# Kernel tuning notes

Hardware: AMD Instinct MI355X
Metric: run time of the kernel (lower is better)

The kernel has to match this reference:

```python
import jax, jax.numpy as jnp
import numpy as np

CORR = 5          # corr_size (patch_size)
UP = 2            # upsample_param
CH = [512, 1024, 512, 256, 256, 256]
SZ = [64, 32, 16, 8, 4, 2]   # pyramid spatial sizes; UP*2**i upsamples all to 128
B = 2
P = CORR * CORR

def upsample_nearest(x, f):
    # nn.Upsample(scale_factor=f, mode='nearest') for integer f
    return jnp.repeat(jnp.repeat(x, f, axis=2), f, axis=3)

def correlate(f1, f2):
    # spatial_correlation_sample: kernel=1, patch=CORR, stride=1, padding=0, dilation_patch=1
    # out[b, pi*CORR+pj, y, x] = sum_c f1[b,c,y,x] * f2[b,c,y+pi-r,x+pj-r] (zeros out of range)
    r = CORR // 2
    b, c, h, w = f1.shape
    f2p = jnp.pad(f2, ((0, 0), (0, 0), (r, r), (r, r)))
    outs = []
    for pi in range(CORR):
        for pj in range(CORR):
            sh = jax.lax.dynamic_slice(f2p, (0, 0, pi, pj), (b, c, h, w))
            outs.append(jnp.sum(f1 * sh, axis=1))
    return jnp.stack(outs, axis=1)  # [B, P, h, w]

def avgpool(x):
    # AvgPool2d(kernel_size=3, stride=2, padding=1), count_include_pad=True (torch default)
    s = jax.lax.reduce_window(x, 0.0, jax.lax.add, (1, 1, 3, 3), (1, 1, 2, 2), ((0, 0), (0, 0), (1, 1), (1, 1)))
    return s / 9.0

def conv3x3(x, w, b):
    y = jax.lax.conv_general_dilated(x, w, (1, 1), ((1, 1), (1, 1)), dimension_numbers=("NCHW", "OIHW", "NCHW"))
    return y + b[None, :, None, None]

def level_step(feat1, feat2, h_pre, c_pre, w, b, lvl):
    f = UP * (2 ** lvl)
    u1 = upsample_nearest(feat1, f)
    u2 = upsample_nearest(feat2, f)
    corr = jax.nn.leaky_relu(correlate(u1, u2), 0.01)
    # int(log2(up_W / feat_W)) pools; this is <= 6 so only avg_pooling1 is ever used
    for _ in range(int(np.log2(u1.shape[3] // feat1.shape[3]))):
        corr = avgpool(corr)
    gates = conv3x3(jnp.concatenate([corr, h_pre], axis=1), w, b)
    i = jax.nn.sigmoid(gates[:, :P])
    fg = jax.nn.sigmoid(gates[:, P:2 * P])
    o = jax.nn.sigmoid(gates[:, 2 * P:3 * P])
    g = jnp.tanh(gates[:, 3 * P:])
    c_next = fg * c_pre + i * g
    h_next = o * jnp.tanh(c_next)
    return h_next, c_next

def setup_inputs():
    keys = jax.random.split(jax.random.key(0), 40)
    d = {}
    k = 0
    for i in range(6):
        d[f"x{i}"] = jax.random.normal(keys[k], (B, CH[i], SZ[i], SZ[i]), jnp.float32); k += 1
        d[f"xp{i}"] = jax.random.normal(keys[k], (B, CH[i], SZ[i], SZ[i]), jnp.float32); k += 1
        d[f"h{i}"] = jax.random.normal(keys[k], (B, P, SZ[i], SZ[i]), jnp.float32); k += 1
        d[f"c{i}"] = jax.random.normal(keys[k], (B, P, SZ[i], SZ[i]), jnp.float32); k += 1
    for i in range(6):
        d[f"W{i}"] = jax.random.normal(keys[k], (4 * P, 2 * P, 3, 3), jnp.float32) * 0.05; k += 1
        d[f"b{i}"] = jnp.zeros((4 * P,), jnp.float32)
    return d

def reference(x0, x1, x2, x3, x4, x5, xp0, xp1, xp2, xp3, xp4, xp5,
              h0, h1, h2, h3, h4, h5, c0, c1, c2, c3, c4, c5,
              W0, W1, W2, W3, W4, W5, b0, b1, b2, b3, b4, b5):
    xs = [x0, x1, x2, x3, x4, x5]
    xps = [xp0, xp1, xp2, xp3, xp4, xp5]
    hs = [h0, h1, h2, h3, h4, h5]
    cs = [c0, c1, c2, c3, c4, c5]
    Ws = [W0, W1, W2, W3, W4, W5]
    bs = [b0, b1, b2, b3, b4, b5]
    outs = []
    for lvl in range(6):
        h_next, c_next = level_step(xs[lvl], xps[lvl], hs[lvl], cs[lvl], Ws[lvl], bs[lvl], lvl)
        outs.extend([h_next, c_next])
    return tuple(outs)
```

## Files before the change

### kernel.cpp

```cpp
#include <hip/hip_runtime.h>

#define NB 2
#define PP 25
#define NLVL 6

struct Params {
  const float* x1[NLVL];
  const float* x2[NLVL];
  const float* h[NLVL];
  const float* c[NLVL];
  const float* W[NLVL];
  const float* bias[NLVL];
  float* Dpart[NLVL];
  float* D[NLVL];
  float* pooled[NLVL];
  float* WT[NLVL];
  float* hout[NLVL];
  float* cout[NLVL];
};

__device__ __forceinline__ float lrelu(float v) { return v > 0.f ? v : 0.01f * v; }

__global__ __launch_bounds__(256) void repack_kernel(Params pr) {
  const int lvl = blockIdx.y;
  const float* W = pr.W[lvl];
  float* WT = pr.WT[lvl];
  for (int i = blockIdx.x * 256 + threadIdx.x; i < 100 * 450; i += gridDim.x * 256) {
    const int oc = i / 450;
    const int r = i - oc * 450;
    WT[r * 100 + oc] = W[i];
  }
}

__global__ __launch_bounds__(256) void dcorr_kernel(Params pr) {
  static const int SZt[6] = {64, 32, 16, 8, 4, 2};
  static const int CHt[6] = {512, 1024, 512, 256, 256, 256};
  static const int NCH[6] = {16, 16, 4, 1, 1, 1};
  static const int LGQ[6] = {4, 3, 2, 0, 0, 0};
  const int lvl = blockIdx.y;
  const int S = SZt[lvl], C = CHt[lvl], nch = NCH[lvl];
  const int rows = NB * S;
  const int bid = blockIdx.x;
  if (bid >= rows * nch) return;
  const int row = bid / nch;
  const int chunk = bid - row * nch;
  const int b = row / S, yb = row - b * S;
  const int tid = threadIdx.x;
  const size_t nlev = (size_t)NB * S * S * 9;
  float* part = pr.Dpart[lvl] + (size_t)chunk * nlev;

  __shared__ float red[9216];

  if (S >= 16) {
    const int lgq = LGQ[lvl];
    const int xqn = S >> 2;
    const int cgn = 256 >> lgq;
    const int xq = tid & (xqn - 1);
    const int cg = tid >> lgq;
    const int chpc = C / nch;
    const int cpt = chpc / cgn;
    const int xb0 = xq << 2;

    const float* f1b = pr.x1[lvl] + (size_t)b * C * S * S + (size_t)yb * S + xb0;
    const float* f2b = pr.x2[lvl] + (size_t)b * C * S * S;

    float acc[9][4];
#pragma unroll
    for (int jj = 0; jj < 9; ++jj)
#pragma unroll
      for (int j = 0; j < 4; ++j) acc[jj][j] = 0.f;

    const int c0 = chunk * chpc + cg;
    for (int t = 0; t < cpt; ++t) {
      const int cc = c0 + t * cgn;
      const float4 f1 = *(const float4*)(f1b + (size_t)cc * S * S);
      const float f1a[4] = {f1.x, f1.y, f1.z, f1.w};
      const float* p2 = f2b + (size_t)cc * S * S;
#pragma unroll
      for (int dy = 0; dy < 3; ++dy) {
        const int yy = yb + dy - 1;
        if (yy < 0 || yy >= S) continue;
        const float* prow = p2 + (size_t)yy * S;
        const float4 m = *(const float4*)(prow + xb0);
        const float lm = (xb0 > 0) ? prow[xb0 - 1] : 0.f;
        const float rm = (xb0 + 4 < S) ? prow[xb0 + 4] : 0.f;
        const float wl[4] = {lm, m.x, m.y, m.z};
        const float wc[4] = {m.x, m.y, m.z, m.w};
        const float wr[4] = {m.y, m.z, m.w, rm};
#pragma unroll
        for (int j = 0; j < 4; ++j) {
          acc[dy * 3 + 0][j] = fmaf(f1a[j], wl[j], acc[dy * 3 + 0][j]);
          acc[dy * 3 + 1][j] = fmaf(f1a[j], wc[j], acc[dy * 3 + 1][j]);
          acc[dy * 3 + 2][j] = fmaf(f1a[j], wr[j], acc[dy * 3 + 2][j]);
        }
      }
    }

    const int n = S * 9;
#pragma unroll
    for (int jj = 0; jj < 9; ++jj)
#pragma unroll
      for (int j = 0; j < 4; ++j)
        red[cg * n + (xb0 + j) * 9 + jj] = acc[jj][j];
    __syncthreads();
    for (int g = cgn >> 1; g >= 1; g >>= 1) {
      for (int i = tid; i < g * n; i += 256) {
        const int c = i / n, e = i - c * n;
        red[c * n + e] += red[(c + g) * n + e];
      }
      __syncthreads();
    }
    float* out = part + (size_t)(b * S + yb) * S * 9;
    for (int i = tid; i < n; i += 256) out[i] = red[i];
  } else {
    const int lg = (S == 8) ? 3 : ((S == 4) ? 2 : 1);
    const int xb = tid & (S - 1), cg = tid >> lg;
    const int NG = 256 >> lg;
    const int cpt = C / NG;

    const float* f1base = pr.x1[lvl] + (size_t)b * C * S * S + (size_t)yb * S + xb;
    const float* f2base = pr.x2[lvl] + (size_t)b * C * S * S;

    float acc[9];
#pragma unroll
    for (int j = 0; j < 9; ++j) acc[j] = 0.f;

    for (int t = 0; t < cpt; ++t) {
      const int cc = cg + t * NG;
      const float f1 = f1base[(size_t)cc * S * S];
      const float* p2 = f2base + (size_t)cc * S * S;
#pragma unroll
      for (int dy = 0; dy < 3; ++dy) {
        const int yy = yb + dy - 1;
        if (yy < 0 || yy >= S) continue;
        const float* prow = p2 + yy * S;
#pragma unroll
        for (int dx = 0; dx < 3; ++dx) {
          const int xx = xb + dx - 1;
          const float v = (xx >= 0 && xx < S) ? prow[xx] : 0.f;
          acc[dy * 3 + dx] += f1 * v;
        }
      }
    }

#pragma unroll
    for (int j = 0; j < 9; ++j) red[tid * 9 + j] = acc[j];
    __syncthreads();
    for (int g = NG >> 1; g >= 1; g >>= 1) {
      if (cg < g) {
#pragma unroll
        for (int j = 0; j < 9; ++j) red[tid * 9 + j] += red[(tid + g * S) * 9 + j];
      }
      __syncthreads();
    }
    if (cg == 0) {
      float* Dp = part + ((size_t)(b * S + yb) * S + xb) * 9;
#pragma unroll
      for (int j = 0; j < 9; ++j) Dp[j] = red[tid * 9 + j];
    }
  }
}

__global__ __launch_bounds__(256) void dreduce_kernel(Params pr) {
  static const int SZt[6] = {64, 32, 16, 8, 4, 2};
  static const int NCH[6] = {16, 16, 4, 1, 1, 1};
  const int lvl = blockIdx.y;
  const int S = SZt[lvl], nch = NCH[lvl];
  const int n = NB * S * S * 9;
  const int i = blockIdx.x * 256 + threadIdx.x;
  if (i >= n) return;
  const float* part = pr.Dpart[lvl];
  float s = 0.f;
  for (int c = 0; c < nch; ++c) s += part[(size_t)c * n + i];
  pr.D[lvl][i] = lrelu(s);
}

__global__ __launch_bounds__(256) void pool_kernel(Params pr) {
  static const int SZt[6] = {64, 32, 16, 8, 4, 2};
  static const int NYC[6] = {8, 4, 2, 1, 1, 1};
  static const int LGS[6] = {6, 5, 4, 3, 2, 1};
  const int lvl = blockIdx.y;
  const int S = SZt[lvl], k = lvl + 1, f = 1 << k, nyc = NYC[lvl], lgS = LGS[lvl];
  const int nyo = S / nyc;
  const int bid = blockIdx.x;
  if (bid >= 50 * nyc) return;
  const int yc = bid / 50;
  const int bp = bid - yc * 50;
  const int b = bp / 25, p = bp - (bp / 25) * 25;
  const int dpy = p / 5 - 2, dpx = p - (p / 5) * 5 - 2;
  const int tid = threadIdx.x;
  const int yo0 = yc * nyo;

  __shared__ float ckb[2][130], clb[2][66];
  __shared__ float Dl[5184];
  __shared__ float tmp[1024];

  if (tid == 0) { ckb[0][0] = 1.f; clb[0][0] = 1.f; }
  __syncthreads();
  int rj = 0, cur = 0;
  for (int j = 0; j < k; ++j) {
    const int half = 1 << j, rn = 2 * half - 1;
    float cknew = 0.f, clnew = 0.f;
    if (tid <= 2 * rn) {
      const int t = tid - rn;
#pragma unroll
      for (int e = -1; e <= 1; ++e) {
        const int u = t + e * half;
        if (u >= -rj && u <= rj) cknew += ckb[cur][u + rj];
      }
      cknew *= (1.f / 3.f);
    }
    if (tid < 2 * half) {
      const int y = tid;
      float s = (y < half) ? clb[cur][y] : 0.f;
      const int u = y - half;
      if (u >= -rj && u <= rj) s += ckb[cur][u + rj];
      clnew = s * (1.f / 3.f);
    }
    __syncthreads();
    if (tid <= 2 * rn) ckb[cur ^ 1][tid] = cknew;
    if (tid < 2 * half) clb[cur ^ 1][tid] = clnew;
    __syncthreads();
    cur ^= 1;
    rj = rn;
  }
  const float* ck = ckb[cur];
  const float* cl = clb[cur];

  const int yb0 = (yo0 > 0) ? yo0 - 1 : 0;
  const int nyb = (yo0 + nyo - 1) - yb0 + 1;
  const float* Dg = pr.D[lvl] + (size_t)b * S * S * 9 + (size_t)yb0 * S * 9;
  const int nload = nyb * S * 9;
  for (int i = tid; i < nload; i += 256) Dl[i] = Dg[i];
  __syncthreads();

  for (int item = tid; item < nyo * 128; item += 256) {
    const int yol = item >> 7, x = item & 127;
    const int yo = yo0 + yol;
    const int xb = x >> k, tx = x & (f - 1);
    const int txp = tx + dpx;
    const int dxi = (txp < 0) ? 0 : ((txp >= f) ? 2 : 1);
    float sum = 0.f;
    if (yo == 0) {
      for (int y = 0; y < f; ++y) {
        const int typ = y + dpy;
        const int dyi = (typ < 0) ? 0 : ((typ >= f) ? 2 : 1);
        sum += cl[y] * Dl[((0 - yb0) * S + xb) * 9 + dyi * 3 + dxi];
      }
    } else {
      const int ylo = yo * f - (f - 1);
      for (int t = 0; t < 2 * f - 1; ++t) {
        const int y = ylo + t;
        const int yb = y >> k, ty = y & (f - 1);
        const int typ = ty + dpy;
        const int dyi = (typ < 0) ? 0 : ((typ >= f) ? 2 : 1);
        sum += ck[t] * Dl[((yb - yb0) * S + xb) * 9 + dyi * 3 + dxi];
      }
    }
    tmp[yol * 128 + x] = sum;
  }
  __syncthreads();

  float* out = pr.pooled[lvl] + (size_t)(b * PP + p) * S * S;
  for (int item = tid; item < nyo * S; item += 256) {
    const int yol = item >> lgS, xo = item & (S - 1);
    float sum = 0.f;
    if (xo == 0) {
      for (int x = 0; x < f; ++x) sum += cl[x] * tmp[yol * 128 + x];
    } else {
      const int xlo = xo * f - (f - 1);
      for (int t = 0; t < 2 * f - 1; ++t) sum += ck[t] * tmp[yol * 128 + xlo + t];
    }
    out[(size_t)(yo0 + yol) * S + xo] = sum;
  }
}

__global__ __launch_bounds__(256) void conv_kernel(Params pr) {
  static const int SZt[6] = {64, 32, 16, 8, 4, 2};
  static const int XTt[6] = {16, 16, 16, 8, 4, 2};
  static const int NXGt[6] = {2, 2, 2, 1, 1, 1};
  const int lvl = blockIdx.y;
  const int S = SZt[lvl], xtile = XTt[lvl], nxg = NXGt[lvl];
  const int nxt = S / xtile;
  const int nblk = NB * S * nxt;
  const int bid = blockIdx.x;
  if (bid >= nblk) return;
  const int b = bid / (S * nxt);
  const int rem = bid - b * (S * nxt);
  const int y = rem / nxt;
  const int xt = rem - y * nxt;
  const int xb0 = xt * xtile;
  const int tid = threadIdx.x;
  const int icc = tid >> 6;
  const int sub = tid & 63;
  const int nact = 25 * nxg;

  __shared__ float lds[7232];

  {
    const float* pooled = pr.pooled[lvl] + (size_t)b * PP * S * S;
    const float* hin = pr.h[lvl] + (size_t)b * PP * S * S;
    for (int i = tid; i < 150 * 20; i += 256) {
      const int r = i / 20, j = i - r * 20;
      const int ky = r / 50, ic = r - ky * 50;
      const int yy = y + ky - 1;
      const int x = xb0 + j - 1;
      float v = 0.f;
      if (yy >= 0 && yy < S && x >= 0 && x < S && j < xtile + 2)
        v = (ic < PP) ? pooled[((size_t)ic * S + yy) * S + x]
                      : hin[((size_t)(ic - PP) * S + yy) * S + x];
      lds[r * 20 + j] = v;
    }
  }
  __syncthreads();

  float acc[4][8];
#pragma unroll
  for (int q = 0; q < 4; ++q)
#pragma unroll
    for (int xx = 0; xx < 8; ++xx) acc[q][xx] = 0.f;

  if (sub < nact) {
    const int xg = sub / 25;
    const int p = sub - xg * 25;
    const int xoff = xg * 8;
    const int ic0 = (icc * 50) >> 2;
    const int ic1 = ((icc + 1) * 50) >> 2;
    const float* wbase = pr.WT[lvl] + p;

    float w[4][9], wn[4][9];
#pragma unroll
    for (int q = 0; q < 4; ++q)
#pragma unroll
      for (int t = 0; t < 9; ++t) w[q][t] = wbase[((size_t)ic0 * 9 + t) * 100 + q * 25];

    for (int ic = ic0; ic < ic1; ++ic) {
      const bool pre = (ic + 1 < ic1);
      if (pre) {
        const float* wq = wbase + (size_t)(ic + 1) * 900;
#pragma unroll
        for (int q = 0; q < 4; ++q)
#pragma unroll
          for (int t = 0; t < 9; ++t) wn[q][t] = wq[t * 100 + q * 25];
      }
#pragma unroll
      for (int ky = 0; ky < 3; ++ky) {
        const float4* rp = (const float4*)(lds + (ky * 50 + ic) * 20 + xoff);
        const float4 A = rp[0], Bv = rp[1], Cv = rp[2];
        const float sg[12] = {A.x, A.y, A.z, A.w, Bv.x, Bv.y, Bv.z, Bv.w,
                              Cv.x, Cv.y, Cv.z, Cv.w};
#pragma unroll
        for (int q = 0; q < 4; ++q) {
          const float w0 = w[q][ky * 3], w1 = w[q][ky * 3 + 1], w2 = w[q][ky * 3 + 2];
#pragma unroll
          for (int xx = 0; xx < 8; ++xx)
            acc[q][xx] = fmaf(w0, sg[xx], fmaf(w1, sg[xx + 1], fmaf(w2, sg[xx + 2], acc[q][xx])));
        }
      }
      if (pre) {
#pragma unroll
        for (int q = 0; q < 4; ++q)
#pragma unroll
          for (int t = 0; t < 9; ++t) w[q][t] = wn[q][t];
      }
    }
  }
  __syncthreads();

  if (sub < nact) {
    float* slot = lds + (icc * 50 + sub) * 36;
#pragma unroll
    for (int q = 0; q < 4; ++q) {
      ((float4*)slot)[q * 2] = make_float4(acc[q][0], acc[q][1], acc[q][2], acc[q][3]);
      ((float4*)slot)[q * 2 + 1] = make_float4(acc[q][4], acc[q][5], acc[q][6], acc[q][7]);
    }
  }
  __syncthreads();

  if (tid < nact) {
    const int xg2 = tid / 25;
    const int p2 = tid - xg2 * 25;
    const int xoff2 = xg2 * 8;

    float g4[4][8];
#pragma unroll
    for (int q = 0; q < 4; ++q)
#pragma unroll
      for (int xx = 0; xx < 8; ++xx) {
        float s = 0.f;
#pragma unroll
        for (int k2 = 0; k2 < 4; ++k2) s += lds[(k2 * 50 + tid) * 36 + q * 8 + xx];
        g4[q][xx] = s;
      }

    const float bi = pr.bias[lvl][p2];
    const float bf = pr.bias[lvl][p2 + 25];
    const float bo = pr.bias[lvl][p2 + 50];
    const float bg = pr.bias[lvl][p2 + 75];
    const size_t base = ((size_t)(b * PP + p2) * S + y) * S + xb0 + xoff2;
    const float* cin = pr.c[lvl] + base;
    float* ho = pr.hout[lvl] + base;
    float* co = pr.cout[lvl] + base;

    float cp[8], hn[8], cn[8];
    if (S >= 8) {
      const float4 c0 = ((const float4*)cin)[0];
      const float4 c1 = ((const float4*)cin)[1];
      cp[0] = c0.x; cp[1] = c0.y; cp[2] = c0.z; cp[3] = c0.w;
      cp[4] = c1.x; cp[5] = c1.y; cp[6] = c1.z; cp[7] = c1.w;
    } else {
#pragma unroll
      for (int xx = 0; xx < 8; ++xx) cp[xx] = (xx < S) ? cin[xx] : 0.f;
    }
#pragma unroll
    for (int xx = 0; xx < 8; ++xx) {
      const float gi = g4[0][xx] + bi;
      const float gf = g4[1][xx] + bf;
      const float go = g4[2][xx] + bo;
      const float gg = g4[3][xx] + bg;
      const float i_ = 1.f / (1.f + __expf(-gi));
      const float f_ = 1.f / (1.f + __expf(-gf));
      const float o_ = 1.f / (1.f + __expf(-go));
      const float g_ = 1.f - 2.f / (__expf(2.f * gg) + 1.f);
      const float c_ = f_ * cp[xx] + i_ * g_;
      const float t2 = 1.f - 2.f / (__expf(2.f * c_) + 1.f);
      cn[xx] = c_;
      hn[xx] = o_ * t2;
    }
    if (S >= 8) {
      ((float4*)ho)[0] = make_float4(hn[0], hn[1], hn[2], hn[3]);
      ((float4*)ho)[1] = make_float4(hn[4], hn[5], hn[6], hn[7]);
      ((float4*)co)[0] = make_float4(cn[0], cn[1], cn[2], cn[3]);
      ((float4*)co)[1] = make_float4(cn[4], cn[5], cn[6], cn[7]);
    } else {
#pragma unroll
      for (int xx = 0; xx < 8; ++xx)
        if (xx < S) { ho[xx] = hn[xx]; co[xx] = cn[xx]; }
    }
  }
}

extern "C" void kernel_launch(void* const* d_in, const int* in_sizes, int n_in,
                              void* d_out, int out_size, void* d_ws, size_t ws_size,
                              hipStream_t stream) {
  static const int SZ[NLVL] = {64, 32, 16, 8, 4, 2};
  static const int NCH[NLVL] = {16, 16, 4, 1, 1, 1};

  Params pr;
  float* ws = (float*)d_ws;
  size_t off = 0;
  for (int l = 0; l < NLVL; ++l) {
    pr.Dpart[l] = ws + off;
    off += (size_t)NCH[l] * NB * SZ[l] * SZ[l] * 9;
  }
  for (int l = 0; l < NLVL; ++l) { pr.D[l] = ws + off; off += (size_t)NB * SZ[l] * SZ[l] * 9; }
  for (int l = 0; l < NLVL; ++l) { pr.pooled[l] = ws + off; off += (size_t)NB * PP * SZ[l] * SZ[l]; }
  for (int l = 0; l < NLVL; ++l) { pr.WT[l] = ws + off; off += 100 * 450; }

  float* out = (float*)d_out;
  size_t ooff = 0;
  for (int l = 0; l < NLVL; ++l) {
    pr.hout[l] = out + ooff; ooff += (size_t)NB * PP * SZ[l] * SZ[l];
    pr.cout[l] = out + ooff; ooff += (size_t)NB * PP * SZ[l] * SZ[l];
  }

  for (int l = 0; l < NLVL; ++l) {
    pr.x1[l] = (const float*)d_in[4 * l + 0];
    pr.x2[l] = (const float*)d_in[4 * l + 1];
    pr.h[l]  = (const float*)d_in[4 * l + 2];
    pr.c[l]  = (const float*)d_in[4 * l + 3];
    pr.W[l]    = (const float*)d_in[24 + 2 * l];
    pr.bias[l] = (const float*)d_in[25 + 2 * l];
  }

  repack_kernel<<<dim3(45, NLVL), 256, 0, stream>>>(pr);
  dcorr_kernel<<<dim3(2048, NLVL), 256, 0, stream>>>(pr);
  dreduce_kernel<<<dim3(288, NLVL), 256, 0, stream>>>(pr);
  pool_kernel<<<dim3(400, NLVL), 256, 0, stream>>>(pr);
  conv_kernel<<<dim3(512, NLVL), 256, 0, stream>>>(pr);
}
```

Before: 242.9 us.

## Split levels 0-1 correlation into fine channel chunks without shared reduction

For the two largest levels, the correlation kernel now gives each thread 8 channels and a 4-wide x strip, so every block handles one channel chunk over a tile of rows. Each thread writes its 3x3 partial sums straight to the partial buffer, with no shared-memory tree reduction. This moves the channel reduction into dreduce_kernel, which now reads float4 vectors over many more chunks (64 and 128). The aim is to drop the syncthreads reduction overhead and cut the dcorr grid, at the cost of more partial-buffer traffic and a heavier reduce pass.

```diff
diff --git a/kernel.cpp b/kernel.cpp
--- a/kernel.cpp
+++ b/kernel.cpp
@@ -35,24 +35,98 @@
 __global__ __launch_bounds__(256) void dcorr_kernel(Params pr) {
   static const int SZt[6] = {64, 32, 16, 8, 4, 2};
   static const int CHt[6] = {512, 1024, 512, 256, 256, 256};
-  static const int NCH[6] = {16, 16, 4, 1, 1, 1};
-  static const int LGQ[6] = {4, 3, 2, 0, 0, 0};
+  static const int NCH[6] = {64, 128, 4, 1, 1, 1};
   const int lvl = blockIdx.y;
   const int S = SZt[lvl], C = CHt[lvl], nch = NCH[lvl];
+  const int bid = blockIdx.x;
+  const int tid = threadIdx.x;
+  const size_t nlev = (size_t)NB * S * S * 9;
+
+  if (lvl <= 1) {
+    int b, y, chunk, xq;
+    if (lvl == 0) {
+      chunk = bid & 63;
+      const int rest = bid >> 6;
+      const int yt = rest & 3;
+      b = rest >> 2;
+      xq = tid & 15;
+      y = yt * 16 + (tid >> 4);
+    } else {
+      if (bid >= 256) return;
+      chunk = bid & 127;
+      b = bid >> 7;
+      xq = tid & 7;
+      y = tid >> 3;
+    }
+    const int xb0 = xq << 2;
+    const int c0 = chunk * 8;
+
+    const float* f1b = pr.x1[lvl] + (((size_t)b * C + c0) * S + y) * S + xb0;
+    const float* f2b = pr.x2[lvl] + ((size_t)b * C + c0) * S * S;
+
+    float acc[9][4];
+#pragma unroll
+    for (int jj = 0; jj < 9; ++jj)
+#pragma unroll
+      for (int j = 0; j < 4; ++j) acc[jj][j] = 0.f;
+
+#pragma unroll
+    for (int t = 0; t < 8; ++t) {
+      const float4 f1 = *(const float4*)(f1b + (size_t)t * S * S);
+      const float f1a[4] = {f1.x, f1.y, f1.z, f1.w};
+      const float* p2 = f2b + (size_t)t * S * S;
+#pragma unroll
+      for (int dy = 0; dy < 3; ++dy) {
+        const int yy = y + dy - 1;
+        const bool yok = (yy >= 0) && (yy < S);
+        const float* prow = p2 + (size_t)yy * S;
+        float4 m;
+        float lm, rm;
+        if (yok) {
+          m = *(const float4*)(prow + xb0);
+          lm = (xb0 > 0) ? prow[xb0 - 1] : 0.f;
+          rm = (xb0 + 4 < S) ? prow[xb0 + 4] : 0.f;
+        } else {
+          m = make_float4(0.f, 0.f, 0.f, 0.f);
+          lm = 0.f;
+          rm = 0.f;
+        }
+        const float wl[4] = {lm, m.x, m.y, m.z};
+        const float wc[4] = {m.x, m.y, m.z, m.w};
+        const float wr[4] = {m.y, m.z, m.w, rm};
+#pragma unroll
+        for (int j = 0; j < 4; ++j) {
+          acc[dy * 3 + 0][j] = fmaf(f1a[j], wl[j], acc[dy * 3 + 0][j]);
+          acc[dy * 3 + 1][j] = fmaf(f1a[j], wc[j], acc[dy * 3 + 1][j]);
+          acc[dy * 3 + 2][j] = fmaf(f1a[j], wr[j], acc[dy * 3 + 2][j]);
+        }
+      }
+    }
+
+    float4 buf4[9];
+    float* buf = (float*)buf4;
+#pragma unroll
+    for (int j = 0; j < 4; ++j)
+#pragma unroll
+      for (int jj = 0; jj < 9; ++jj) buf[j * 9 + jj] = acc[jj][j];
+    float* out = pr.Dpart[lvl] + (size_t)chunk * nlev +
+                 ((size_t)(b * S + y) * S + xb0) * 9;
+#pragma unroll
+    for (int v = 0; v < 9; ++v) ((float4*)out)[v] = buf4[v];
+    return;
+  }
+
   const int rows = NB * S;
-  const int bid = blockIdx.x;
   if (bid >= rows * nch) return;
   const int row = bid / nch;
   const int chunk = bid - row * nch;
   const int b = row / S, yb = row - b * S;
-  const int tid = threadIdx.x;
-  const size_t nlev = (size_t)NB * S * S * 9;
   float* part = pr.Dpart[lvl] + (size_t)chunk * nlev;
 
   __shared__ float red[9216];
 
   if (S >= 16) {
-    const int lgq = LGQ[lvl];
+    const int lgq = 2;
     const int xqn = S >> 2;
     const int cgn = 256 >> lgq;
     const int xq = tid & (xqn - 1);
@@ -163,16 +237,21 @@
 
 __global__ __launch_bounds__(256) void dreduce_kernel(Params pr) {
   static const int SZt[6] = {64, 32, 16, 8, 4, 2};
-  static const int NCH[6] = {16, 16, 4, 1, 1, 1};
+  static const int NCH[6] = {64, 128, 4, 1, 1, 1};
   const int lvl = blockIdx.y;
   const int S = SZt[lvl], nch = NCH[lvl];
-  const int n = NB * S * S * 9;
-  const int i = blockIdx.x * 256 + threadIdx.x;
-  if (i >= n) return;
-  const float* part = pr.Dpart[lvl];
-  float s = 0.f;
-  for (int c = 0; c < nch; ++c) s += part[(size_t)c * n + i];
-  pr.D[lvl][i] = lrelu(s);
+  const int n4 = (NB * S * S * 9) >> 2;
+  const int i4 = blockIdx.x * 256 + threadIdx.x;
+  if (i4 >= n4) return;
+  const float4* part = (const float4*)pr.Dpart[lvl];
+  float4 s = make_float4(0.f, 0.f, 0.f, 0.f);
+  for (int c = 0; c < nch; ++c) {
+    const float4 v = part[(size_t)c * n4 + i4];
+    s.x += v.x; s.y += v.y; s.z += v.z; s.w += v.w;
+  }
+  float4 o;
+  o.x = lrelu(s.x); o.y = lrelu(s.y); o.z = lrelu(s.z); o.w = lrelu(s.w);
+  ((float4*)pr.D[lvl])[i4] = o;
 }
 
 __global__ __launch_bounds__(256) void pool_kernel(Params pr) {
@@ -444,7 +523,7 @@
                               void* d_out, int out_size, void* d_ws, size_t ws_size,
                               hipStream_t stream) {
   static const int SZ[NLVL] = {64, 32, 16, 8, 4, 2};
-  static const int NCH[NLVL] = {16, 16, 4, 1, 1, 1};
+  static const int NCH[NLVL] = {64, 128, 4, 1, 1, 1};
 
   Params pr;
   float* ws = (float*)d_ws;
@@ -474,8 +553,8 @@
   }
 
   repack_kernel<<<dim3(45, NLVL), 256, 0, stream>>>(pr);
-  dcorr_kernel<<<dim3(2048, NLVL), 256, 0, stream>>>(pr);
-  dreduce_kernel<<<dim3(288, NLVL), 256, 0, stream>>>(pr);
+  dcorr_kernel<<<dim3(512, NLVL), 256, 0, stream>>>(pr);
+  dreduce_kernel<<<dim3(72, NLVL), 256, 0, stream>>>(pr);
   pool_kernel<<<dim3(400, NLVL), 256, 0, stream>>>(pr);
   conv_kernel<<<dim3(512, NLVL), 256, 0, stream>>>(pr);
 }
```

New measurement: 268.5 us. 10.6% more time.
